# Kernel tuning notes

Hardware: AMD Instinct MI355X
Metric: run time of the kernel (lower is better)

## Reference

```python
import jax, jax.numpy as jnp
import numpy as np

D_IN, E, K = 128, 256, 16
LN_EPS = 1e-5


def _layernorm(h, g, b):
    mu = jnp.mean(h, axis=-1, keepdims=True)
    var = jnp.mean(jnp.square(h - mu), axis=-1, keepdims=True)
    return (h - mu) * jax.lax.rsqrt(var + LN_EPS) * g + b


def _gelu(h):
    return jax.nn.gelu(h, approximate=False)  # torch F.gelu default = exact erf


def setup_inputs() -> dict:
    key = jax.random.key(0)
    ks = jax.random.split(key, 8)
    B, N = 8, 2048
    def lin(k, fan_in, fan_out):
        bound = 1.0 / np.sqrt(fan_in)
        return jax.random.uniform(k, (fan_in, fan_out), jnp.float32, -bound, bound)
    return {
        "x": jax.random.normal(ks[0], (B, N, D_IN), jnp.float32),
        "coordinates": jax.random.normal(ks[1], (B, N, 3), jnp.float32),
        "W1": lin(ks[2], 2 * D_IN, E), "b1": jnp.zeros((E,), jnp.float32),
        "g1": jnp.ones((E,), jnp.float32), "be1": jnp.zeros((E,), jnp.float32),
        "W2": lin(ks[3], E, E), "b2": jnp.zeros((E,), jnp.float32),
        "g2": jnp.ones((E,), jnp.float32), "be2": jnp.zeros((E,), jnp.float32),
        "W3": lin(ks[4], E, E), "b3": jnp.zeros((E,), jnp.float32),
        "g3": jnp.ones((E,), jnp.float32), "be3": jnp.zeros((E,), jnp.float32),
        "Ws": lin(ks[5], D_IN, E), "bs": jnp.zeros((E,), jnp.float32),
    }


def reference(x, coordinates, W1, b1, g1, be1, W2, b2, g2, be2, W3, b3, g3, be3, Ws, bs):
    B, N, D = x.shape
    # --- dynamic kNN graph: squared euclidean distances (sqrt is monotone, skip it) ---
    sq = jnp.sum(coordinates * coordinates, axis=-1)                 # [B,N]
    d2 = sq[:, :, None] + sq[:, None, :] - 2.0 * jnp.einsum(
        'bnc,bmc->bnm', coordinates, coordinates)                    # [B,N,N]
    d2 = jnp.maximum(d2, 0.0)
    _, idx = jax.lax.top_k(-d2, K)                                   # [B,N,K] nearest (incl. self)
    # --- gather neighbor features: neighbors[b,n,j] = x[b, idx[b,n,j]] ---
    neighbors = jax.vmap(lambda xb, ib: xb[ib])(x, idx)              # [B,N,K,D]
    central = jnp.broadcast_to(x[:, :, None, :], (B, N, K, D))       # [B,N,K,D]
    edge = jnp.concatenate([central, neighbors - central], axis=-1)  # [B,N,K,2D]
    # --- edge MLP: (Linear -> LN -> GELU) x3 ---
    h = _gelu(_layernorm(edge @ W1 + b1, g1, be1))
    h = _gelu(_layernorm(h @ W2 + b2, g2, be2))
    h = _gelu(_layernorm(h @ W3 + b3, g3, be3))                      # [B,N,K,E]
    # --- max aggregate over neighbors + shortcut ---
    agg = jnp.max(h, axis=2)                                         # [B,N,E]
    return _gelu(agg + x @ Ws + bs)
```

## Files before the change

### kernel.cpp

```cpp
#include <hip/hip_runtime.h>
#include <hip/hip_bf16.h>
#include <math.h>

#define B_ 8
#define N_ 2048
#define D_ 128
#define E_ 256
#define K_ 16
#define LN_EPS 1e-5f

typedef short bf16x8 __attribute__((ext_vector_type(8)));
typedef float f32x4 __attribute__((ext_vector_type(4)));
typedef float f32x2 __attribute__((ext_vector_type(2)));

__device__ __forceinline__ float sq3_ref(float x, float y, float z) {
#pragma clang fp contract(off)
    float s = x * x + y * y;
    s = s + z * z;
    return s;
}
__device__ __forceinline__ float d2_ref(float qx, float qy, float qz, float sqq,
                                        float mx, float my, float mz, float sqm) {
#pragma clang fp contract(off)
    float dot = mx * qx + my * qy;
    dot = dot + mz * qz;
    float t1 = sqq + sqm;
    float t2 = 2.0f * dot;
    float d2 = t1 - t2;
    return d2 > 0.0f ? d2 : 0.0f;
}

__device__ __forceinline__ unsigned pack2(float a, float b) {
    union { __hip_bfloat162 h2; unsigned u; } cv;
    cv.h2 = __float22bfloat162_rn(float2{a, b});
    return cv.u;
}

__device__ __forceinline__ f32x2 gelu2(f32x2 v) {
    const f32x2 w = v * v;
    f32x2 inner = w * 0.044715f;
    inner.x += 1.0f; inner.y += 1.0f;
    const f32x2 ue = (v * -2.3022083f) * inner;
    f32x2 t;
    t.x = __builtin_amdgcn_exp2f(ue.x);
    t.y = __builtin_amdgcn_exp2f(ue.y);
    f32x2 den = t;
    den.x += 1.0f; den.y += 1.0f;
    f32x2 r;
    r.x = __builtin_amdgcn_rcpf(den.x);
    r.y = __builtin_amdgcn_rcpf(den.y);
    return v * r;
}

__device__ __forceinline__ float dpp_rowmax16(float v) {
    int x = __float_as_int(v);
    v = fmaxf(v, __int_as_float(__builtin_amdgcn_mov_dpp(x, 0xB1, 0xF, 0xF, true)));
    x = __float_as_int(v);
    v = fmaxf(v, __int_as_float(__builtin_amdgcn_mov_dpp(x, 0x4E, 0xF, 0xF, true)));
    x = __float_as_int(v);
    v = fmaxf(v, __int_as_float(__builtin_amdgcn_mov_dpp(x, 0x141, 0xF, 0xF, true)));
    x = __float_as_int(v);
    v = fmaxf(v, __int_as_float(__builtin_amdgcn_mov_dpp(x, 0x140, 0xF, 0xF, true)));
    return v;
}

__global__ __launch_bounds__(512) void knn_select_kernel(const float* __restrict__ coords,
                                                         int* __restrict__ knn_out) {
    __shared__ float lc[3][N_];
    __shared__ float lsq[N_];
    __shared__ int cnt[8];
    const int wave = threadIdx.x >> 6;
    const int lane = threadIdx.x & 63;
    const int p = blockIdx.x * 8 + wave;
    const int b = p >> 11;
    const int n0 = p & (N_ - 1);
    const float* cb = coords + (size_t)b * N_ * 3;
    for (int i = threadIdx.x; i < N_ * 3; i += 512) {
        int n = i / 3, c = i - 3 * n;
        lc[c][n] = cb[i];
    }
    __syncthreads();
    for (int n = threadIdx.x; n < N_; n += 512) lsq[n] = sq3_ref(lc[0][n], lc[1][n], lc[2][n]);
    __syncthreads();

    const float qx = lc[0][n0], qy = lc[1][n0], qz = lc[2][n0], sqq = lsq[n0];
    unsigned key[32];
#pragma unroll
    for (int j = 0; j < 32; ++j) {
        const int m = j * 64 + lane;
        key[j] = __float_as_uint(d2_ref(qx, qy, qz, sqq, lc[0][m], lc[1][m], lc[2][m], lsq[m]));
    }

    unsigned prefix = 0;
    int rem = K_, setc = N_, bshift = 0;
    bool bounded = false;
    for (int bit = 31; bit >= 0; --bit) {
        const unsigned want = prefix << 1;
        int c = 0;
#pragma unroll
        for (int j = 0; j < 32; ++j) c += ((key[j] >> bit) == want) ? 1 : 0;
        for (int off = 1; off < 64; off <<= 1) c += __shfl_xor(c, off, 64);
        if (rem <= c) { prefix = want; setc = c; }
        else          { prefix = want | 1u; rem -= c; setc -= c; }
        bshift = bit;
        if (setc == rem) { bounded = true; break; }
    }

    if (lane == 0) cnt[wave] = 0;
    int* op = knn_out + (size_t)p * K_;
    const unsigned long long BE = bounded ? (((unsigned long long)prefix + 1ull) << bshift)
                                          : (unsigned long long)prefix;
#pragma unroll
    for (int j = 0; j < 32; ++j) {
        if ((unsigned long long)key[j] < BE) {
            int s = atomicAdd(&cnt[wave], 1);
            op[s] = j * 64 + lane;
        }
    }
    if (!bounded) {
        const unsigned V = prefix;
#pragma unroll
        for (int j = 0; j < 32; ++j) {
            if (rem > 0) {
                unsigned long long mask = __ballot(key[j] == V);
                int below = __popcll(mask & ((1ull << lane) - 1ull));
                if (key[j] == V && below < rem) {
                    int s = atomicAdd(&cnt[wave], 1);
                    op[s] = j * 64 + lane;
                }
                rem -= __popcll(mask);
            }
        }
    }
}

__global__ __launch_bounds__(64) void wprep_kernel(const float* __restrict__ W1,
                                                   const float* __restrict__ W2,
                                                   const float* __restrict__ W3,
                                                   const float* __restrict__ Ws,
                                                   short* __restrict__ WF) {
    const int bi = blockIdx.x;
    const int lane = threadIdx.x;
    const int g = lane >> 4, e = lane & 15;
    const float* W;
    int mt, kt;
    if (bi < 384) {
        const int L = bi >> 7;
        const int t = bi & 127;
        kt = t >> 4; mt = t & 15;
        W = (L == 0) ? W1 : (L == 1) ? W2 : W3;
    } else {
        const int t = bi - 384;
        kt = t >> 4; mt = t & 15;
        W = Ws;
    }
    const int f = 16 * mt + e;
    unsigned v[4];
#pragma unroll
    for (int i2 = 0; i2 < 4; ++i2) {
        const int k = 32 * kt + 8 * g + 2 * i2;
        v[i2] = pack2(W[(size_t)k * E_ + f], W[(size_t)(k + 1) * E_ + f]);
    }
    uint4 u; u.x = v[0]; u.y = v[1]; u.z = v[2]; u.w = v[3];
    *reinterpret_cast<uint4*>(WF + ((size_t)bi * 64 + lane) * 8) = u;
}

__global__ __launch_bounds__(256) void shortcut_kernel(const float* __restrict__ x,
                                                       const short* __restrict__ WF,
                                                       const float* __restrict__ bs,
                                                       float* __restrict__ out) {
    const int wave = threadIdx.x >> 6;
    const int lane = threadIdx.x & 63;
    const int e = lane & 15;
    const int g = lane >> 4;
    const int p0 = (blockIdx.x * 4 + wave) * 16;
    const float* xr = x + (size_t)(p0 + e) * D_;
    const short* WSF = WF + (size_t)(24 * 16) * 512;

    f32x4 acc[16];
    const f32x4 z4 = {0.f, 0.f, 0.f, 0.f};
#pragma unroll
    for (int mt = 0; mt < 16; ++mt) acc[mt] = z4;

#pragma unroll
    for (int kt = 0; kt < 4; ++kt) {
        const float4 xa = *(const float4*)(xr + kt * 32 + g * 8);
        const float4 xb = *(const float4*)(xr + kt * 32 + g * 8 + 4);
        union { unsigned u[4]; bf16x8 v; } bx;
        bx.u[0] = pack2(xa.x, xa.y); bx.u[1] = pack2(xa.z, xa.w);
        bx.u[2] = pack2(xb.x, xb.y); bx.u[3] = pack2(xb.z, xb.w);
#pragma unroll
        for (int mt = 0; mt < 16; ++mt) {
            const bf16x8 a = *(const bf16x8*)(WSF + ((size_t)(kt * 16 + mt) * 64 + lane) * 8);
            acc[mt] = __builtin_amdgcn_mfma_f32_16x16x32_bf16(a, bx.v, acc[mt], 0, 0, 0);
        }
    }
#pragma unroll
    for (int mt = 0; mt < 16; ++mt) {
        const float4 bsv = *(const float4*)(bs + 16 * mt + 4 * g);
        float4 o;
        o.x = acc[mt][0] + bsv.x; o.y = acc[mt][1] + bsv.y;
        o.z = acc[mt][2] + bsv.z; o.w = acc[mt][3] + bsv.w;
        *(float4*)(out + (size_t)(p0 + e) * E_ + 16 * mt + 4 * g) = o;
    }
}

#define WCHUNKS 24

__device__ __forceinline__ void stage_chunk(const short* __restrict__ WF,
                                            short* __restrict__ dst,
                                            int c, int wave, int lane) {
    const short* src = WF + ((size_t)(c << 4) << 9);
#pragma unroll
    for (int i = 0; i < 4; ++i) {
        const int slot = (i << 8) + (wave << 6);
        const short* gp = src + ((size_t)(slot + lane) << 3);
        short* lp = dst + ((size_t)slot << 3);
        __builtin_amdgcn_global_load_lds(
            (const __attribute__((address_space(1))) void*)gp,
            (__attribute__((address_space(3))) void*)lp, 16, 0, 0);
    }
}

__global__ __launch_bounds__(256, 2) void edgeconv_mfma(
    const float* __restrict__ x, const int* __restrict__ knn,
    const short* __restrict__ WF,
    const float* __restrict__ b1, const float* __restrict__ g1, const float* __restrict__ be1,
    const float* __restrict__ b2, const float* __restrict__ g2, const float* __restrict__ be2,
    const float* __restrict__ b3, const float* __restrict__ g3, const float* __restrict__ be3,
    float* __restrict__ out)
{
    __shared__ short Hl[2][2][4096];
    __shared__ short Wbuf[2][8192];
    __shared__ float4 Xch[2][2][16];
    __shared__ float Pl[9 * 256];
    const int tid  = threadIdx.x;
    const int wave = tid >> 6;
    const int lane = tid & 63;
    const int wq = wave & 1;
    const int pr = wave >> 1;
    const int e = lane & 15;
    const int g = lane >> 4;
    const int p = blockIdx.x * 4 + wave;
    const int b = p >> 11;
    const int n = p & (N_ - 1);
    const unsigned swz = (unsigned)((e & 7) << 4);
    char* Hown = (char*)&Hl[pr][wq][0];
    char* Hp0  = (char*)&Hl[pr][0][0];
    char* Hp1  = (char*)&Hl[pr][1][0];

    stage_chunk(WF, &Wbuf[0][0], 0, wave, lane);

    {
        const float* srcs[9] = {b1, g1, be1, b2, g2, be2, b3, g3, be3};
#pragma unroll
        for (int a = 0; a < 9; ++a) Pl[a * 256 + tid] = srcs[a][tid];
    }

    {
        const float4* xr = (const float4*)(x + ((size_t)b * N_ + n) * D_);
        const int nb = knn[(size_t)p * K_ + e];
        const float4* nr = (const float4*)(x + ((size_t)b * N_ + nb) * D_);
#pragma unroll
        for (int c2 = 0; c2 < 8; ++c2) {
            const float4 cv = xr[8 * g + c2];
            const float4 nv = nr[8 * g + c2];
            const int base = (e << 9) + (g << 6) + (c2 << 3);
            *(uint2*)(Hown + (base ^ swz)) = make_uint2(pack2(cv.x, cv.y), pack2(cv.z, cv.w));
            *(uint2*)(Hown + ((base + 256) ^ swz)) =
                make_uint2(pack2(nv.x - cv.x, nv.y - cv.y), pack2(nv.z - cv.z, nv.w - cv.w));
        }
    }

    f32x4 acc0[8], acc1[8];
    int pb = 0;
    const f32x4 z4 = {0.f, 0.f, 0.f, 0.f};

    for (int L = 0; L < 3; ++L) {
        const float* PlL = &Pl[L * 768];
#pragma unroll
        for (int mtl = 0; mtl < 8; ++mtl) { acc0[mtl] = z4; acc1[mtl] = z4; }

        for (int kt = 0; kt < 8; ++kt) {
            const int c = L * 8 + kt;
            asm volatile("s_waitcnt vmcnt(0)" ::: "memory");
            __syncthreads();
            if (c + 1 < WCHUNKS) stage_chunk(WF, &Wbuf[pb ^ 1][0], c + 1, wave, lane);
            const int offB = (int)((unsigned)((e << 9) + (kt << 6) + (g << 4)) ^ swz);
            const bf16x8 Bc0 = *(const bf16x8*)(Hp0 + offB);
            const bf16x8 Bc1 = *(const bf16x8*)(Hp1 + offB);
            const short* Wc = &Wbuf[pb][0];
            __builtin_amdgcn_s_setprio(1);
#pragma unroll
            for (int mtl = 0; mtl < 8; ++mtl) {
                const bf16x8 a = *(const bf16x8*)(Wc + ((((wq << 3) + mtl) << 6) + lane) * 8);
                acc0[mtl] = __builtin_amdgcn_mfma_f32_16x16x32_bf16(a, Bc0, acc0[mtl], 0, 0, 0);
                acc1[mtl] = __builtin_amdgcn_mfma_f32_16x16x32_bf16(a, Bc1, acc1[mtl], 0, 0, 0);
            }
            __builtin_amdgcn_s_setprio(0);
            pb ^= 1;
        }

        f32x2 s2_0 = {0.f, 0.f}, q2_0 = {0.f, 0.f};
        f32x2 s2_1 = {0.f, 0.f}, q2_1 = {0.f, 0.f};
#pragma unroll
        for (int mtl = 0; mtl < 8; ++mtl) {
            const int mtg = (wq << 3) + mtl;
            const float4 bv = *(const float4*)(PlL + mtg * 16 + (g << 2));
            const f32x2 blo = {bv.x, bv.y}, bhi = {bv.z, bv.w};
            f32x2 a0lo = {acc0[mtl][0], acc0[mtl][1]};
            f32x2 a0hi = {acc0[mtl][2], acc0[mtl][3]};
            f32x2 a1lo = {acc1[mtl][0], acc1[mtl][1]};
            f32x2 a1hi = {acc1[mtl][2], acc1[mtl][3]};
            a0lo = a0lo + blo; a0hi = a0hi + bhi;
            a1lo = a1lo + blo; a1hi = a1hi + bhi;
            s2_0 = s2_0 + a0lo; s2_0 = s2_0 + a0hi;
            q2_0 = q2_0 + a0lo * a0lo; q2_0 = q2_0 + a0hi * a0hi;
            s2_1 = s2_1 + a1lo; s2_1 = s2_1 + a1hi;
            q2_1 = q2_1 + a1lo * a1lo; q2_1 = q2_1 + a1hi * a1hi;
            acc0[mtl][0] = a0lo.x; acc0[mtl][1] = a0lo.y;
            acc0[mtl][2] = a0hi.x; acc0[mtl][3] = a0hi.y;
            acc1[mtl][0] = a1lo.x; acc1[mtl][1] = a1lo.y;
            acc1[mtl][2] = a1hi.x; acc1[mtl][3] = a1hi.y;
        }
        float s0 = s2_0.x + s2_0.y, q0 = q2_0.x + q2_0.y;
        float s1 = s2_1.x + s2_1.y, q1 = q2_1.x + q2_1.y;
        s0 += __shfl_xor(s0, 16, 64); s0 += __shfl_xor(s0, 32, 64);
        q0 += __shfl_xor(q0, 16, 64); q0 += __shfl_xor(q0, 32, 64);
        s1 += __shfl_xor(s1, 16, 64); s1 += __shfl_xor(s1, 32, 64);
        q1 += __shfl_xor(q1, 16, 64); q1 += __shfl_xor(q1, 32, 64);
        if (lane < 16) Xch[pr][wq][e] = make_float4(s0, q0, s1, q1);
        __syncthreads();
        const float4 oX = Xch[pr][wq ^ 1][e];
        const float mu0 = (s0 + oX.x) * (1.0f / 256.0f);
        const float var0 = fmaf(-mu0, mu0, (q0 + oX.y) * (1.0f / 256.0f));
        const float rstd0 = rsqrtf(var0 + LN_EPS);
        const float mu1 = (s1 + oX.z) * (1.0f / 256.0f);
        const float var1 = fmaf(-mu1, mu1, (q1 + oX.w) * (1.0f / 256.0f));
        const float rstd1 = rsqrtf(var1 + LN_EPS);

#pragma unroll
        for (int mtl = 0; mtl < 8; ++mtl) {
            const int mtg = (wq << 3) + mtl;
            const float4 gv  = *(const float4*)(PlL + 256 + mtg * 16 + (g << 2));
            const float4 bev = *(const float4*)(PlL + 512 + mtg * 16 + (g << 2));
            const f32x2 glo = {gv.x, gv.y}, ghi = {gv.z, gv.w};
            const f32x2 belo = {bev.x, bev.y}, behi = {bev.z, bev.w};
            const f32x2 A0lo = glo * rstd0, A0hi = ghi * rstd0;
            const f32x2 C0lo = A0lo * (-mu0) + belo, C0hi = A0hi * (-mu0) + behi;
            const f32x2 v0lo = {acc0[mtl][0], acc0[mtl][1]};
            const f32x2 v0hi = {acc0[mtl][2], acc0[mtl][3]};
            const f32x2 r0lo = gelu2(v0lo * A0lo + C0lo);
            const f32x2 r0hi = gelu2(v0hi * A0hi + C0hi);
            const f32x2 A1lo = glo * rstd1, A1hi = ghi * rstd1;
            const f32x2 C1lo = A1lo * (-mu1) + belo, C1hi = A1hi * (-mu1) + behi;
            const f32x2 v1lo = {acc1[mtl][0], acc1[mtl][1]};
            const f32x2 v1hi = {acc1[mtl][2], acc1[mtl][3]};
            const f32x2 r1lo = gelu2(v1lo * A1lo + C1lo);
            const f32x2 r1hi = gelu2(v1hi * A1hi + C1hi);
            if (L < 2) {
                const int wb = (int)((unsigned)((e << 9) + (mtg << 5) + (g << 3)) ^ swz);
                *(uint2*)(Hp0 + wb) = make_uint2(pack2(r0lo.x, r0lo.y), pack2(r0hi.x, r0hi.y));
                *(uint2*)(Hp1 + wb) = make_uint2(pack2(r1lo.x, r1lo.y), pack2(r1hi.x, r1hi.y));
            } else {
                acc0[mtl][0] = r0lo.x; acc0[mtl][1] = r0lo.y;
                acc0[mtl][2] = r0hi.x; acc0[mtl][3] = r0hi.y;
                acc1[mtl][0] = r1lo.x; acc1[mtl][1] = r1lo.y;
                acc1[mtl][2] = r1hi.x; acc1[mtl][3] = r1hi.y;
            }
        }
    }

#pragma unroll
    for (int mtl = 0; mtl < 8; ++mtl) {
#pragma unroll
        for (int i = 0; i < 4; ++i) {
            acc0[mtl][i] = dpp_rowmax16(acc0[mtl][i]);
            acc1[mtl][i] = dpp_rowmax16(acc1[mtl][i]);
        }
    }
    float* Sb0 = (float*)Hp0;
    float* Sb1 = (float*)Hp1;
#pragma unroll
    for (int mtl = 0; mtl < 8; ++mtl) {
        if (e == mtl) {
            const int fo = (((wq << 3) + mtl) << 4) + (g << 2);
            *(float4*)(Sb0 + fo) = *(const float4*)&acc0[mtl];
            *(float4*)(Sb1 + fo) = *(const float4*)&acc1[mtl];
        }
    }
    __syncthreads();

    const int f0 = 16 * e + (g << 2);
    const float* SbO = wq ? Sb1 : Sb0;
    const float4 agg = *(const float4*)(SbO + f0);
    float* op = out + (size_t)p * E_ + f0;
    const float4 ssc = *(const float4*)op;
    f32x2 elo = {agg.x + ssc.x, agg.y + ssc.y};
    f32x2 ehi = {agg.z + ssc.z, agg.w + ssc.w};
    const f32x2 olo = gelu2(elo);
    const f32x2 ohi = gelu2(ehi);
    float4 o;
    o.x = olo.x; o.y = olo.y; o.z = ohi.x; o.w = ohi.y;
    *(float4*)op = o;
}

extern "C" void kernel_launch(void* const* d_in, const int* in_sizes, int n_in,
                              void* d_out, int out_size, void* d_ws, size_t ws_size,
                              hipStream_t stream) {
    const float* x      = (const float*)d_in[0];
    const float* coords = (const float*)d_in[1];
    const float* W1  = (const float*)d_in[2];
    const float* b1  = (const float*)d_in[3];
    const float* g1  = (const float*)d_in[4];
    const float* be1 = (const float*)d_in[5];
    const float* W2  = (const float*)d_in[6];
    const float* b2  = (const float*)d_in[7];
    const float* g2  = (const float*)d_in[8];
    const float* be2 = (const float*)d_in[9];
    const float* W3  = (const float*)d_in[10];
    const float* b3  = (const float*)d_in[11];
    const float* g3  = (const float*)d_in[12];
    const float* be3 = (const float*)d_in[13];
    const float* Ws  = (const float*)d_in[14];
    const float* bs  = (const float*)d_in[15];
    float* out = (float*)d_out;

    int*   knn = (int*)d_ws;
    short* WF  = (short*)((char*)d_ws + (1 << 20));

    wprep_kernel<<<448, 64, 0, stream>>>(W1, W2, W3, Ws, WF);
    knn_select_kernel<<<B_ * (N_ / 8), 512, 0, stream>>>(coords, knn);
    shortcut_kernel<<<(B_ * N_) / 64, 256, 0, stream>>>(x, WF, bs, out);
    edgeconv_mfma<<<(B_ * N_) / 4, 256, 0, stream>>>(
        x, knn, WF, b1, g1, be1, b2, g2, be2, b3, g3, be3, out);
}
```

Before: 330.2 us.

## Merge kNN and weight-prep kernels; single-buffer weight staging and drop param LDS copy

Fuses the weight-packing kernel into the kNN selection kernel as extra blocks of one launch, removing a kernel launch. In the edge MLP kernel, the double-buffered async weight staging becomes a single buffer that is loaded and waited on synchronously each k-step. Bias and LayerNorm parameters are now read from global memory instead of being copied into LDS, and the occupancy hint of 2 is dropped from the launch bounds. Together these cut LDS use, which may raise occupancy, but they give up the overlap between weight loads and MFMA work and add a barrier per k-step.

Result: slower. 354.6 us (+7.4%).

```diff
diff --git a/kernel.cpp b/kernel.cpp
--- a/kernel.cpp
+++ b/kernel.cpp
@@ -64,105 +64,109 @@
     return v;
 }
 
-__global__ __launch_bounds__(512) void knn_select_kernel(const float* __restrict__ coords,
-                                                         int* __restrict__ knn_out) {
-    __shared__ float lc[3][N_];
-    __shared__ float lsq[N_];
-    __shared__ int cnt[8];
-    const int wave = threadIdx.x >> 6;
-    const int lane = threadIdx.x & 63;
-    const int p = blockIdx.x * 8 + wave;
-    const int b = p >> 11;
-    const int n0 = p & (N_ - 1);
-    const float* cb = coords + (size_t)b * N_ * 3;
-    for (int i = threadIdx.x; i < N_ * 3; i += 512) {
-        int n = i / 3, c = i - 3 * n;
-        lc[c][n] = cb[i];
-    }
-    __syncthreads();
-    for (int n = threadIdx.x; n < N_; n += 512) lsq[n] = sq3_ref(lc[0][n], lc[1][n], lc[2][n]);
-    __syncthreads();
-
-    const float qx = lc[0][n0], qy = lc[1][n0], qz = lc[2][n0], sqq = lsq[n0];
-    unsigned key[32];
-#pragma unroll
-    for (int j = 0; j < 32; ++j) {
-        const int m = j * 64 + lane;
-        key[j] = __float_as_uint(d2_ref(qx, qy, qz, sqq, lc[0][m], lc[1][m], lc[2][m], lsq[m]));
-    }
-
-    unsigned prefix = 0;
-    int rem = K_, setc = N_, bshift = 0;
-    bool bounded = false;
-    for (int bit = 31; bit >= 0; --bit) {
-        const unsigned want = prefix << 1;
-        int c = 0;
-#pragma unroll
-        for (int j = 0; j < 32; ++j) c += ((key[j] >> bit) == want) ? 1 : 0;
-        for (int off = 1; off < 64; off <<= 1) c += __shfl_xor(c, off, 64);
-        if (rem <= c) { prefix = want; setc = c; }
-        else          { prefix = want | 1u; rem -= c; setc -= c; }
-        bshift = bit;
-        if (setc == rem) { bounded = true; break; }
-    }
-
-    if (lane == 0) cnt[wave] = 0;
-    int* op = knn_out + (size_t)p * K_;
-    const unsigned long long BE = bounded ? (((unsigned long long)prefix + 1ull) << bshift)
-                                          : (unsigned long long)prefix;
-#pragma unroll
-    for (int j = 0; j < 32; ++j) {
-        if ((unsigned long long)key[j] < BE) {
-            int s = atomicAdd(&cnt[wave], 1);
-            op[s] = j * 64 + lane;
-        }
-    }
-    if (!bounded) {
-        const unsigned V = prefix;
+__global__ __launch_bounds__(512) void prep_kernel(
+    const float* __restrict__ coords,
+    const float* __restrict__ W1, const float* __restrict__ W2,
+    const float* __restrict__ W3, const float* __restrict__ Ws,
+    int* __restrict__ knn_out, short* __restrict__ WF)
+{
+    __shared__ float smem[4 * N_ + 8];
+    const int bid = blockIdx.x;
+    const int tid = threadIdx.x;
+
+    if (bid < 2048) {
+        float (*lc)[N_] = (float(*)[N_])smem;
+        float* lsq = smem + 3 * N_;
+        int* cnt = (int*)(smem + 4 * N_);
+        const int wave = tid >> 6;
+        const int lane = tid & 63;
+        const int p = bid * 8 + wave;
+        const int b = p >> 11;
+        const int n0 = p & (N_ - 1);
+        const float* cb = coords + (size_t)b * N_ * 3;
+        for (int i = tid; i < N_ * 3; i += 512) {
+            int n = i / 3, c = i - 3 * n;
+            lc[c][n] = cb[i];
+        }
+        __syncthreads();
+        for (int n = tid; n < N_; n += 512) lsq[n] = sq3_ref(lc[0][n], lc[1][n], lc[2][n]);
+        __syncthreads();
+
+        const float qx = lc[0][n0], qy = lc[1][n0], qz = lc[2][n0], sqq = lsq[n0];
+        unsigned key[32];
 #pragma unroll
         for (int j = 0; j < 32; ++j) {
-            if (rem > 0) {
-                unsigned long long mask = __ballot(key[j] == V);
-                int below = __popcll(mask & ((1ull << lane) - 1ull));
-                if (key[j] == V && below < rem) {
-                    int s = atomicAdd(&cnt[wave], 1);
-                    op[s] = j * 64 + lane;
+            const int m = j * 64 + lane;
+            key[j] = __float_as_uint(d2_ref(qx, qy, qz, sqq, lc[0][m], lc[1][m], lc[2][m], lsq[m]));
+        }
+
+        unsigned prefix = 0;
+        int rem = K_, setc = N_, bshift = 0;
+        bool bounded = false;
+        for (int bit = 31; bit >= 0; --bit) {
+            const unsigned want = prefix << 1;
+            int c = 0;
+#pragma unroll
+            for (int j = 0; j < 32; ++j) c += ((key[j] >> bit) == want) ? 1 : 0;
+            for (int off = 1; off < 64; off <<= 1) c += __shfl_xor(c, off, 64);
+            if (rem <= c) { prefix = want; setc = c; }
+            else          { prefix = want | 1u; rem -= c; setc -= c; }
+            bshift = bit;
+            if (setc == rem) { bounded = true; break; }
+        }
+
+        if (lane == 0) cnt[wave] = 0;
+        int* op = knn_out + (size_t)p * K_;
+        const unsigned long long BE = bounded ? (((unsigned long long)prefix + 1ull) << bshift)
+                                              : (unsigned long long)prefix;
+#pragma unroll
+        for (int j = 0; j < 32; ++j) {
+            if ((unsigned long long)key[j] < BE) {
+                int s = atomicAdd(&cnt[wave], 1);
+                op[s] = j * 64 + lane;
+            }
+        }
+        if (!bounded) {
+            const unsigned V = prefix;
+#pragma unroll
+            for (int j = 0; j < 32; ++j) {
+                if (rem > 0) {
+                    unsigned long long mask = __ballot(key[j] == V);
+                    int below = __popcll(mask & ((1ull << lane) - 1ull));
+                    if (key[j] == V && below < rem) {
+                        int s = atomicAdd(&cnt[wave], 1);
+                        op[s] = j * 64 + lane;
+                    }
+                    rem -= __popcll(mask);
                 }
-                rem -= __popcll(mask);
             }
         }
-    }
-}
-
-__global__ __launch_bounds__(64) void wprep_kernel(const float* __restrict__ W1,
-                                                   const float* __restrict__ W2,
-                                                   const float* __restrict__ W3,
-                                                   const float* __restrict__ Ws,
-                                                   short* __restrict__ WF) {
-    const int bi = blockIdx.x;
-    const int lane = threadIdx.x;
-    const int g = lane >> 4, e = lane & 15;
-    const float* W;
-    int mt, kt;
-    if (bi < 384) {
-        const int L = bi >> 7;
-        const int t = bi & 127;
-        kt = t >> 4; mt = t & 15;
-        W = (L == 0) ? W1 : (L == 1) ? W2 : W3;
     } else {
-        const int t = bi - 384;
-        kt = t >> 4; mt = t & 15;
-        W = Ws;
-    }
-    const int f = 16 * mt + e;
-    unsigned v[4];
-#pragma unroll
-    for (int i2 = 0; i2 < 4; ++i2) {
-        const int k = 32 * kt + 8 * g + 2 * i2;
-        v[i2] = pack2(W[(size_t)k * E_ + f], W[(size_t)(k + 1) * E_ + f]);
-    }
-    uint4 u; u.x = v[0]; u.y = v[1]; u.z = v[2]; u.w = v[3];
-    *reinterpret_cast<uint4*>(WF + ((size_t)bi * 64 + lane) * 8) = u;
+        const int unit = (bid - 2048) * 8 + (tid >> 6);
+        const int lane = tid & 63;
+        const int g = lane >> 4, e = lane & 15;
+        const float* W;
+        int mt, kt;
+        if (unit < 384) {
+            const int L = unit >> 7;
+            const int t = unit & 127;
+            kt = t >> 4; mt = t & 15;
+            W = (L == 0) ? W1 : (L == 1) ? W2 : W3;
+        } else {
+            const int t = unit - 384;
+            kt = t >> 4; mt = t & 15;
+            W = Ws;
+        }
+        const int f = 16 * mt + e;
+        unsigned v[4];
+#pragma unroll
+        for (int i2 = 0; i2 < 4; ++i2) {
+            const int k = 32 * kt + 8 * g + 2 * i2;
+            v[i2] = pack2(W[(size_t)k * E_ + f], W[(size_t)(k + 1) * E_ + f]);
+        }
+        uint4 u; u.x = v[0]; u.y = v[1]; u.z = v[2]; u.w = v[3];
+        *reinterpret_cast<uint4*>(WF + ((size_t)unit * 64 + lane) * 8) = u;
+    }
 }
 
 __global__ __launch_bounds__(256) void shortcut_kernel(const float* __restrict__ x,
@@ -205,8 +209,6 @@
     }
 }
 
-#define WCHUNKS 24
-
 __device__ __forceinline__ void stage_chunk(const short* __restrict__ WF,
                                             short* __restrict__ dst,
                                             int c, int wave, int lane) {
@@ -222,7 +224,7 @@
     }
 }
 
-__global__ __launch_bounds__(256, 2) void edgeconv_mfma(
+__global__ __launch_bounds__(256) void edgeconv_mfma(
     const float* __restrict__ x, const int* __restrict__ knn,
     const short* __restrict__ WF,
     const float* __restrict__ b1, const float* __restrict__ g1, const float* __restrict__ be1,
@@ -231,9 +233,8 @@
     float* __restrict__ out)
 {
     __shared__ short Hl[2][2][4096];
-    __shared__ short Wbuf[2][8192];
+    __shared__ short Wbuf[8192];
     __shared__ float4 Xch[2][2][16];
-    __shared__ float Pl[9 * 256];
     const int tid  = threadIdx.x;
     const int wave = tid >> 6;
     const int lane = tid & 63;
@@ -249,14 +250,6 @@
     char* Hp0  = (char*)&Hl[pr][0][0];
     char* Hp1  = (char*)&Hl[pr][1][0];
 
-    stage_chunk(WF, &Wbuf[0][0], 0, wave, lane);
-
-    {
-        const float* srcs[9] = {b1, g1, be1, b2, g2, be2, b3, g3, be3};
-#pragma unroll
-        for (int a = 0; a < 9; ++a) Pl[a * 256 + tid] = srcs[a][tid];
-    }
-
     {
         const float4* xr = (const float4*)(x + ((size_t)b * N_ + n) * D_);
         const int nb = knn[(size_t)p * K_ + e];
@@ -273,32 +266,32 @@
     }
 
     f32x4 acc0[8], acc1[8];
-    int pb = 0;
     const f32x4 z4 = {0.f, 0.f, 0.f, 0.f};
 
     for (int L = 0; L < 3; ++L) {
-        const float* PlL = &Pl[L * 768];
+        const float* bL  = (L == 0) ? b1  : (L == 1) ? b2  : b3;
+        const float* gL  = (L == 0) ? g1  : (L == 1) ? g2  : g3;
+        const float* beL = (L == 0) ? be1 : (L == 1) ? be2 : be3;
 #pragma unroll
         for (int mtl = 0; mtl < 8; ++mtl) { acc0[mtl] = z4; acc1[mtl] = z4; }
 
         for (int kt = 0; kt < 8; ++kt) {
             const int c = L * 8 + kt;
-            asm volatile("s_waitcnt vmcnt(0)" ::: "memory");
             __syncthreads();
-            if (c + 1 < WCHUNKS) stage_chunk(WF, &Wbuf[pb ^ 1][0], c + 1, wave, lane);
             const int offB = (int)((unsigned)((e << 9) + (kt << 6) + (g << 4)) ^ swz);
             const bf16x8 Bc0 = *(const bf16x8*)(Hp0 + offB);
             const bf16x8 Bc1 = *(const bf16x8*)(Hp1 + offB);
-            const short* Wc = &Wbuf[pb][0];
+            stage_chunk(WF, Wbuf, c, wave, lane);
+            asm volatile("s_waitcnt vmcnt(0)" ::: "memory");
+            __syncthreads();
             __builtin_amdgcn_s_setprio(1);
 #pragma unroll
             for (int mtl = 0; mtl < 8; ++mtl) {
-                const bf16x8 a = *(const bf16x8*)(Wc + ((((wq << 3) + mtl) << 6) + lane) * 8);
+                const bf16x8 a = *(const bf16x8*)(Wbuf + ((((wq << 3) + mtl) << 6) + lane) * 8);
                 acc0[mtl] = __builtin_amdgcn_mfma_f32_16x16x32_bf16(a, Bc0, acc0[mtl], 0, 0, 0);
                 acc1[mtl] = __builtin_amdgcn_mfma_f32_16x16x32_bf16(a, Bc1, acc1[mtl], 0, 0, 0);
             }
             __builtin_amdgcn_s_setprio(0);
-            pb ^= 1;
         }
 
         f32x2 s2_0 = {0.f, 0.f}, q2_0 = {0.f, 0.f};
@@ -306,7 +299,7 @@
 #pragma unroll
         for (int mtl = 0; mtl < 8; ++mtl) {
             const int mtg = (wq << 3) + mtl;
-            const float4 bv = *(const float4*)(PlL + mtg * 16 + (g << 2));
+            const float4 bv = *(const float4*)(bL + mtg * 16 + (g << 2));
             const f32x2 blo = {bv.x, bv.y}, bhi = {bv.z, bv.w};
             f32x2 a0lo = {acc0[mtl][0], acc0[mtl][1]};
             f32x2 a0hi = {acc0[mtl][2], acc0[mtl][3]};
@@ -342,8 +335,8 @@
 #pragma unroll
         for (int mtl = 0; mtl < 8; ++mtl) {
             const int mtg = (wq << 3) + mtl;
-            const float4 gv  = *(const float4*)(PlL + 256 + mtg * 16 + (g << 2));
-            const float4 bev = *(const float4*)(PlL + 512 + mtg * 16 + (g << 2));
+            const float4 gv  = *(const float4*)(gL + mtg * 16 + (g << 2));
+            const float4 bev = *(const float4*)(beL + mtg * 16 + (g << 2));
             const f32x2 glo = {gv.x, gv.y}, ghi = {gv.z, gv.w};
             const f32x2 belo = {bev.x, bev.y}, behi = {bev.z, bev.w};
             const f32x2 A0lo = glo * rstd0, A0hi = ghi * rstd0;
@@ -429,8 +422,7 @@
     int*   knn = (int*)d_ws;
     short* WF  = (short*)((char*)d_ws + (1 << 20));
 
-    wprep_kernel<<<448, 64, 0, stream>>>(W1, W2, W3, Ws, WF);
-    knn_select_kernel<<<B_ * (N_ / 8), 512, 0, stream>>>(coords, knn);
+    prep_kernel<<<2048 + 56, 512, 0, stream>>>(coords, W1, W2, W3, Ws, knn, WF);
     shortcut_kernel<<<(B_ * N_) / 64, 256, 0, stream>>>(x, WF, bs, out);
     edgeconv_mfma<<<(B_ * N_) / 4, 256, 0, stream>>>(
         x, knn, WF, b1, g1, be1, b2, g2, be2, b3, g3, be3, out);
```
